# Kernel optimization log

Measured on AMD Instinct MI355X. Metric: run time of the kernel, lower is better.

## Reference

```python
import jax, jax.numpy as jnp
import numpy as np

HIDDEN = 1024
N_HEADS = 16
HEAD_DIM = HIDDEN // N_HEADS


def setup_inputs() -> dict:
    key = jax.random.key(0)
    ks = jax.random.split(key, 8)
    bs, seq = 8, 1024
    hidden_states = jax.random.normal(ks[0], (bs, seq, HIDDEN), dtype=jnp.float32)
    attention_mask = jnp.zeros((bs, 1, 1, seq), dtype=jnp.float32)
    s = 1.0 / np.sqrt(HIDDEN)
    Wq = jax.random.normal(ks[1], (HIDDEN, HIDDEN), dtype=jnp.float32) * s
    bq = jnp.zeros((HIDDEN,), dtype=jnp.float32)
    Wk = jax.random.normal(ks[2], (HIDDEN, HIDDEN), dtype=jnp.float32) * s
    bk = jnp.zeros((HIDDEN,), dtype=jnp.float32)
    Wv = jax.random.normal(ks[3], (HIDDEN, HIDDEN), dtype=jnp.float32) * s
    bv = jnp.zeros((HIDDEN,), dtype=jnp.float32)
    return {"hidden_states": hidden_states, "attention_mask": attention_mask,
            "Wq": Wq, "bq": bq, "Wk": Wk, "bk": bk, "Wv": Wv, "bv": bv}


def _split_heads(x):
    # [b, s, H] -> [b, h, s, d]
    b, s, _ = x.shape
    return x.reshape(b, s, N_HEADS, HEAD_DIM).transpose(0, 2, 1, 3)


def reference(hidden_states, attention_mask, Wq, bq, Wk, bk, Wv, bv):
    q = _split_heads(hidden_states @ Wq.T + bq)
    k = _split_heads(hidden_states @ Wk.T + bk)
    v = _split_heads(hidden_states @ Wv.T + bv)
    scale = 1.0 / np.sqrt(HEAD_DIM).astype(np.float32)
    scores = jnp.einsum('bhqd,bhkd->bhqk', q, k) * scale + attention_mask
    probs = jax.nn.softmax(scores, axis=-1)  # dropout p=0.0 -> identity
    ctx = jnp.einsum('bhqk,bhkd->bhqd', probs, v)
    b, h, s, d = ctx.shape
    return ctx.transpose(0, 2, 1, 3).reshape(b, s, h * d)
```

## Files before the change

kernel.cpp:

```cpp
#include <hip/hip_runtime.h>
#include <stdint.h>
#include <stddef.h>

#define HIDDEN 1024
#define NHEADS 16
#define HDIM   64
#define BS     8
#define SEQ    1024
#define MTOT   (BS*SEQ)
#define QKV_T  ((size_t)MTOT*HIDDEN)

typedef short    bf16x8 __attribute__((ext_vector_type(8)));
typedef short    bf16x4 __attribute__((ext_vector_type(4)));
typedef float    f32x4  __attribute__((ext_vector_type(4)));
typedef uint16_t u16x4  __attribute__((ext_vector_type(4)));

__device__ __forceinline__ uint16_t f2bf(float f) {
  union { float f; uint32_t u; } c; c.f = f;
  uint32_t u = c.u + 0x7FFFu + ((c.u >> 16) & 1u);
  return (uint16_t)(u >> 16);
}

__device__ __forceinline__ uint32_t cvt_pk_bf16(float lo, float hi) {
  uint32_t r;
  asm("v_cvt_pk_bf16_f32 %0, %1, %2" : "=v"(r) : "v"(lo), "v"(hi));
  return r;
}

__device__ __forceinline__ bf16x4 pack_bf16x4(float a, float b, float c, float d) {
  union { uint2 u; bf16x4 v; } cv;
  cv.u.x = cvt_pk_bf16(a, b);
  cv.u.y = cvt_pk_bf16(c, d);
  return cv.v;
}

__device__ __forceinline__ f32x4 mfma_16x16x16(bf16x4 a, bf16x4 b, f32x4 c) {
#if __has_builtin(__builtin_amdgcn_mfma_f32_16x16x16bf16_1k)
  return __builtin_amdgcn_mfma_f32_16x16x16bf16_1k(a, b, c, 0, 0, 0);
#elif __has_builtin(__builtin_amdgcn_mfma_f32_16x16x16_bf16)
  return __builtin_amdgcn_mfma_f32_16x16x16_bf16(a, b, c, 0, 0, 0);
#else
  f32x4 d;
  asm("v_mfma_f32_16x16x16_bf16 %0, %1, %2, %3"
      : "=&v"(d) : "v"(a), "v"(b), "v"(c));
  return d;
#endif
}

__device__ __forceinline__ float exp2fast(float x) {
#if __has_builtin(__builtin_amdgcn_exp2f)
  return __builtin_amdgcn_exp2f(x);
#else
  return __expf(x * 0.69314718056f);
#endif
}

__device__ __forceinline__ void gload_lds16(const uint16_t* g, uint16_t* lds) {
  __builtin_amdgcn_global_load_lds(
      (const __attribute__((address_space(1))) uint32_t*)g,
      (__attribute__((address_space(3))) uint32_t*)lds, 16, 0, 0);
}

__global__ __launch_bounds__(256) void cvt_kernel(
    const float* __restrict__ hs, const float* __restrict__ wq,
    const float* __restrict__ wk, const float* __restrict__ wv,
    uint16_t* __restrict__ hsb, uint16_t* __restrict__ wcat)
{
  const int i4 = blockIdx.x * 256 + threadIdx.x;
  f32x4 v;
  u16x4 o;
  if (i4 < 2097152) {
    v = *((const f32x4*)hs + i4);
    o[0]=f2bf(v[0]); o[1]=f2bf(v[1]); o[2]=f2bf(v[2]); o[3]=f2bf(v[3]);
    *((u16x4*)hsb + i4) = o;
  } else {
    int j4 = i4 - 2097152;
    int w  = j4 >> 18;
    int r4 = j4 & 262143;
    const float* src = (w == 0) ? wq : ((w == 1) ? wk : wv);
    v = *((const f32x4*)src + r4);
    o[0]=f2bf(v[0]); o[1]=f2bf(v[1]); o[2]=f2bf(v[2]); o[3]=f2bf(v[3]);
    *((u16x4*)wcat + j4) = o;
  }
}

__global__ __launch_bounds__(256) void gemm_qkv(
    const uint16_t* __restrict__ hsb, const uint16_t* __restrict__ wcat,
    const float* __restrict__ bq, const float* __restrict__ bk,
    const float* __restrict__ bv, uint16_t* __restrict__ qbuf,
    uint16_t* __restrict__ kbuf, uint16_t* __restrict__ vtbuf)
{
  __shared__ uint16_t Alds[2][128*32];
  __shared__ uint16_t Blds[2][128*32];

  const int bid = blockIdx.x;
  const int wg  = (bid & 7) * 192 + (bid >> 3);
  const int tm  = wg / 24, tn = wg % 24;
  const int m0  = tm * 128, n0 = tn * 128;
  const int t   = threadIdx.x;
  const int l   = t & 63, w = t >> 6;
  const int wm  = w >> 1, wn = w & 1;

  f32x4 acc[4][4];
#pragma unroll
  for (int i = 0; i < 4; i++)
#pragma unroll
    for (int j = 0; j < 4; j++) acc[i][j] = (f32x4){0.f,0.f,0.f,0.f};

  const int r0   = (w * 2) * 16 + (l >> 2);
  const int r1   = (w * 2 + 1) * 16 + (l >> 2);
  const int g0s  = (l & 3) ^ ((r0 >> 1) & 3);
  const int g1s  = (l & 3) ^ ((r1 >> 1) & 3);
  const size_t aoff0 = (size_t)r0 * HIDDEN + g0s * 8;
  const size_t aoff1 = (size_t)r1 * HIDDEN + g1s * 8;

  auto STAGE = [&](int buf, int kt) {
    const uint16_t* Ab = hsb  + (size_t)m0 * HIDDEN + kt * 32;
    const uint16_t* Bb = wcat + (size_t)n0 * HIDDEN + kt * 32;
    gload_lds16(Ab + aoff0, &Alds[buf][(w * 2) * 512]);
    gload_lds16(Ab + aoff1, &Alds[buf][(w * 2 + 1) * 512]);
    gload_lds16(Bb + aoff0, &Blds[buf][(w * 2) * 512]);
    gload_lds16(Bb + aoff1, &Blds[buf][(w * 2 + 1) * 512]);
  };

  auto COMPUTE = [&](int buf) {
    bf16x8 af[4], bfr[4];
    const int G = l >> 4;
#pragma unroll
    for (int i = 0; i < 4; i++) {
      int ar = wm * 64 + i * 16 + (l & 15);
      int gs = (G ^ ((ar >> 1) & 3)) & 3;
      af[i] = *(const bf16x8*)&Alds[buf][ar * 32 + gs * 8];
    }
#pragma unroll
    for (int j = 0; j < 4; j++) {
      int br = wn * 64 + j * 16 + (l & 15);
      int gs = (G ^ ((br >> 1) & 3)) & 3;
      bfr[j] = *(const bf16x8*)&Blds[buf][br * 32 + gs * 8];
    }
#pragma unroll
    for (int i = 0; i < 4; i++)
#pragma unroll
      for (int j = 0; j < 4; j++)
        acc[i][j] = __builtin_amdgcn_mfma_f32_16x16x32_bf16(af[i], bfr[j], acc[i][j], 0, 0, 0);
  };

  STAGE(0, 0);
  STAGE(1, 1);
#pragma unroll 1
  for (int kt = 0; kt < 32; ++kt) {
    if (kt < 31) { asm volatile("s_waitcnt vmcnt(4)" ::: "memory"); }
    else         { asm volatile("s_waitcnt vmcnt(0)" ::: "memory"); }
    __builtin_amdgcn_s_barrier();
    __builtin_amdgcn_sched_barrier(0);
    COMPUTE(kt & 1);
    if (kt < 31) {
      __builtin_amdgcn_s_barrier();
      __builtin_amdgcn_sched_barrier(0);
      if (kt < 30) STAGE(kt & 1, kt + 2);
    }
  }

#pragma unroll
  for (int j = 0; j < 4; j++) {
    int n     = n0 + wn * 64 + j * 16 + (l & 15);
    int which = n >> 10, nn = n & 1023;
    const float* bp = (which == 0) ? bq : ((which == 1) ? bk : bv);
    float bias = bp[nn];
    int hh = nn >> 6, dd = nn & 63;
#pragma unroll
    for (int i = 0; i < 4; i++) {
      if (which == 2) {
        int m_  = m0 + wm * 64 + i * 16 + (l >> 4) * 4;
        int b_  = m_ >> 10, s_ = m_ & 1023;
        size_t bhh = (size_t)(b_ * NHEADS + hh);
        uint2 pk;
        pk.x = cvt_pk_bf16(acc[i][j][0] + bias, acc[i][j][1] + bias);
        pk.y = cvt_pk_bf16(acc[i][j][2] + bias, acc[i][j][3] + bias);
        *(uint2*)&vtbuf[(bhh * HDIM + dd) * SEQ + s_] = pk;
      } else {
#pragma unroll
        for (int r = 0; r < 4; r++) {
          int m  = m0 + wm * 64 + i * 16 + (l >> 4) * 4 + r;
          int b_ = m >> 10, s_ = m & 1023;
          float val = acc[i][j][r] + bias;
          size_t bhh = (size_t)(b_ * NHEADS + hh);
          if (which == 0)
            qbuf[(bhh * SEQ + s_) * HDIM + dd] = f2bf(val * 0.18033688011112042f);
          else
            kbuf[(bhh * SEQ + s_) * HDIM + dd] = f2bf(val);
        }
      }
    }
  }
}

__global__ __launch_bounds__(256) void attn_kernel(
    const uint16_t* __restrict__ qb, const uint16_t* __restrict__ kb,
    const uint16_t* __restrict__ vtb, const float* __restrict__ mask,
    float* __restrict__ out)
{
  __shared__ uint16_t Klds[128 * 64];
  __shared__ uint16_t Vlds[64 * 128];
  __shared__ float    mlds[SEQ];

  const int bid = blockIdx.x;
  const int wg  = (bid & 7) * 128 + (bid >> 3);
  const int bh  = wg >> 3;
  const int qt  = wg & 7;
  const int b   = bh >> 4, h = bh & 15;

  const uint16_t* Qg = qb  + (size_t)bh * SEQ * HDIM;
  const uint16_t* Kg = kb  + (size_t)bh * SEQ * HDIM;
  const uint16_t* Vg = vtb + (size_t)bh * HDIM * SEQ;

  const int t = threadIdx.x, l = t & 63, w = t >> 6;
  const int G = l >> 4, q16 = l & 15;

  for (int i = t; i < SEQ; i += 256)
    mlds[i] = mask[b * SEQ + i] * 1.44269504089f;

  const int q0w = qt * 128 + w * 32;
  bf16x8 qf[2][2];
#pragma unroll
  for (int qi = 0; qi < 2; ++qi)
#pragma unroll
    for (int k0 = 0; k0 < 2; ++k0)
      qf[qi][k0] = *(const bf16x8*)(Qg + (size_t)(q0w + qi * 16 + q16) * HDIM + k0 * 32 + G * 8);

  f32x4 O0[4], O1[4];
#pragma unroll
  for (int dt = 0; dt < 4; dt++) { O0[dt] = (f32x4){0,0,0,0}; O1[dt] = (f32x4){0,0,0,0}; }
  float mrow0 = -3e38f, mrow1 = -3e38f, lrow0 = 0.f, lrow1 = 0.f;

  const int srow8 = l >> 3;
  const int gsrcK = (l & 7) ^ srow8;
  const int qsw = q16 & 7;

  auto softmax_q = [&](f32x4 (&scq)[8], bf16x4 (&paq)[8], float& mq, float& lq,
                       f32x4 (&Oq)[4], int ktbase) {
    float pm = -3e38f;
#pragma unroll
    for (int jn = 0; jn < 8; jn++) {
      f32x4 mvj = *(const f32x4*)&mlds[ktbase + jn * 16 + G * 4];
      scq[jn] += mvj;
      pm = fmaxf(pm, fmaxf(fmaxf(scq[jn][0], scq[jn][1]), fmaxf(scq[jn][2], scq[jn][3])));
    }
    pm = fmaxf(pm, __shfl_xor(pm, 16));
    pm = fmaxf(pm, __shfl_xor(pm, 32));
    if (!__all(pm <= mq + 11.0f)) {
      float mn = fmaxf(mq, pm);
      float fs = exp2fast(mq - mn);
      mq = mn; lq *= fs;
#pragma unroll
      for (int dt = 0; dt < 4; dt++) Oq[dt] *= fs;
    }
    float ps = 0.f;
#pragma unroll
    for (int jn = 0; jn < 8; jn++) {
      float p0 = exp2fast(scq[jn][0] - mq);
      float p1 = exp2fast(scq[jn][1] - mq);
      float p2 = exp2fast(scq[jn][2] - mq);
      float p3 = exp2fast(scq[jn][3] - mq);
      ps += (p0 + p1) + (p2 + p3);
      paq[jn] = pack_bf16x4(p0, p1, p2, p3);
    }
    ps += __shfl_xor(ps, 16);
    ps += __shfl_xor(ps, 32);
    lq += ps;
  };

  __syncthreads();

#pragma unroll 1
  for (int kt = 0; kt < 8; ++kt) {
    const int ktbase = kt * 128;
#pragma unroll
    for (int ja = 0; ja < 4; ja++) {
      const int rbK = ja * 32 + w * 8;
      gload_lds16(Kg + (size_t)(ktbase + rbK + srow8) * HDIM + gsrcK * 8,
                  &Klds[rbK * 64]);
      const int rbV = ja * 16 + w * 4;
      const int dV  = rbV + (l >> 4);
      const int gV  = (l & 15) ^ (dV & 7);
      gload_lds16(Vg + (size_t)dV * SEQ + ktbase + gV * 8,
                  &Vlds[rbV * 128]);
    }
    __syncthreads();

    f32x4 sc0[8], sc1[8];
#pragma unroll
    for (int jn = 0; jn < 8; jn++) {
      const int kr  = jn * 16 + q16;
      const int gs0 = (G ^ qsw) & 7;
      const int gs1 = ((4 + G) ^ qsw) & 7;
      bf16x8 kf0 = *(const bf16x8*)&Klds[kr * 64 + gs0 * 8];
      bf16x8 kf1 = *(const bf16x8*)&Klds[kr * 64 + gs1 * 8];
      f32x4 z = (f32x4){0, 0, 0, 0};
      sc0[jn] = __builtin_amdgcn_mfma_f32_16x16x32_bf16(kf0, qf[0][0], z, 0, 0, 0);
      sc0[jn] = __builtin_amdgcn_mfma_f32_16x16x32_bf16(kf1, qf[0][1], sc0[jn], 0, 0, 0);
      sc1[jn] = __builtin_amdgcn_mfma_f32_16x16x32_bf16(kf0, qf[1][0], z, 0, 0, 0);
      sc1[jn] = __builtin_amdgcn_mfma_f32_16x16x32_bf16(kf1, qf[1][1], sc1[jn], 0, 0, 0);
    }

    bf16x4 pa0[8], pa1[8];
    softmax_q(sc0, pa0, mrow0, lrow0, O0, ktbase);
    softmax_q(sc1, pa1, mrow1, lrow1, O1, ktbase);

#pragma unroll
    for (int jn = 0; jn < 8; jn++) {
      const int gq = 2 * jn + (G >> 1);
#pragma unroll
      for (int dt = 0; dt < 4; dt++) {
        const int dr   = dt * 16 + q16;
        const int slot = gq ^ (dr & 7);
        bf16x4 vf = *(const bf16x4*)&Vlds[dr * 128 + slot * 8 + (G & 1) * 4];
        O0[dt] = mfma_16x16x16(vf, pa0[jn], O0[dt]);
        O1[dt] = mfma_16x16x16(vf, pa1[jn], O1[dt]);
      }
    }
    __syncthreads();
  }

  {
    float inv0 = 1.0f / lrow0, inv1 = 1.0f / lrow1;
    int qa = q0w + q16, qb2 = q0w + 16 + q16;
    float* orow0 = out + (size_t)(b * SEQ + qa)  * HIDDEN + h * HDIM;
    float* orow1 = out + (size_t)(b * SEQ + qb2) * HIDDEN + h * HDIM;
#pragma unroll
    for (int dt = 0; dt < 4; dt++) {
      f32x4 a = O0[dt] * inv0;
      f32x4 c = O1[dt] * inv1;
      *(f32x4*)(orow0 + dt * 16 + G * 4) = a;
      *(f32x4*)(orow1 + dt * 16 + G * 4) = c;
    }
  }
}

extern "C" void kernel_launch(void* const* d_in, const int* in_sizes, int n_in,
                              void* d_out, int out_size, void* d_ws, size_t ws_size,
                              hipStream_t stream) {
  const float* hs   = (const float*)d_in[0];
  const float* mask = (const float*)d_in[1];
  const float* Wq   = (const float*)d_in[2];
  const float* bq   = (const float*)d_in[3];
  const float* Wk   = (const float*)d_in[4];
  const float* bk   = (const float*)d_in[5];
  const float* Wv   = (const float*)d_in[6];
  const float* bv   = (const float*)d_in[7];
  float* out = (float*)d_out;

  uint16_t* hsb  = (uint16_t*)d_ws;
  uint16_t* wcat = (uint16_t*)((char*)d_ws + 16777216u);
  uint16_t* qbuf = (uint16_t*)((char*)d_ws + 23068672u);
  uint16_t* kbuf = (uint16_t*)((char*)d_ws + 39845888u);
  uint16_t* vtbf = (uint16_t*)((char*)d_ws + 56623104u);

  cvt_kernel<<<11264, 256, 0, stream>>>(hs, Wq, Wk, Wv, hsb, wcat);
  gemm_qkv<<<1536, 256, 0, stream>>>(hsb, wcat, bq, bk, bv, qbuf, kbuf, vtbf);
  attn_kernel<<<1024, 256, 0, stream>>>(qbuf, kbuf, vtbf, mask, out);
}
```

Baseline: 144.6 us.

## Enlarge QKV GEMM tile to 256x128 with 512-thread blocks

```diff
diff --git a/kernel.cpp b/kernel.cpp
--- a/kernel.cpp
+++ b/kernel.cpp
@@ -84,22 +84,23 @@
   }
 }
 
-__global__ __launch_bounds__(256) void gemm_qkv(
+__global__ __launch_bounds__(512, 4) void gemm_qkv(
     const uint16_t* __restrict__ hsb, const uint16_t* __restrict__ wcat,
     const float* __restrict__ bq, const float* __restrict__ bk,
     const float* __restrict__ bv, uint16_t* __restrict__ qbuf,
     uint16_t* __restrict__ kbuf, uint16_t* __restrict__ vtbuf)
 {
-  __shared__ uint16_t Alds[2][128*32];
+  __shared__ uint16_t Alds[2][256*32];
   __shared__ uint16_t Blds[2][128*32];
 
   const int bid = blockIdx.x;
-  const int wg  = (bid & 7) * 192 + (bid >> 3);
+  const int wg  = (bid & 7) * 96 + (bid >> 3);
   const int tm  = wg / 24, tn = wg % 24;
-  const int m0  = tm * 128, n0 = tn * 128;
+  const int m0  = tm * 256, n0 = tn * 128;
   const int t   = threadIdx.x;
   const int l   = t & 63, w = t >> 6;
   const int wm  = w >> 1, wn = w & 1;
+  const int q16 = l & 15;
 
   f32x4 acc[4][4];
 #pragma unroll
@@ -107,20 +108,19 @@
 #pragma unroll
     for (int j = 0; j < 4; j++) acc[i][j] = (f32x4){0.f,0.f,0.f,0.f};
 
-  const int r0   = (w * 2) * 16 + (l >> 2);
-  const int r1   = (w * 2 + 1) * 16 + (l >> 2);
-  const int g0s  = (l & 3) ^ ((r0 >> 1) & 3);
-  const int g1s  = (l & 3) ^ ((r1 >> 1) & 3);
-  const size_t aoff0 = (size_t)r0 * HIDDEN + g0s * 8;
-  const size_t aoff1 = (size_t)r1 * HIDDEN + g1s * 8;
+  const int lrow = l >> 2;
+  const int rB   = w * 16 + lrow;
+  const int gsw  = (l & 3) ^ ((rB >> 1) & 3);
+  const size_t offA0 = (size_t)rB * HIDDEN + gsw * 8;
+  const size_t offA1 = (size_t)(128 + rB) * HIDDEN + gsw * 8;
+  const size_t offB  = offA0;
 
   auto STAGE = [&](int buf, int kt) {
     const uint16_t* Ab = hsb  + (size_t)m0 * HIDDEN + kt * 32;
     const uint16_t* Bb = wcat + (size_t)n0 * HIDDEN + kt * 32;
-    gload_lds16(Ab + aoff0, &Alds[buf][(w * 2) * 512]);
-    gload_lds16(Ab + aoff1, &Alds[buf][(w * 2 + 1) * 512]);
-    gload_lds16(Bb + aoff0, &Blds[buf][(w * 2) * 512]);
-    gload_lds16(Bb + aoff1, &Blds[buf][(w * 2 + 1) * 512]);
+    gload_lds16(Ab + offA0, &Alds[buf][(w * 16) * 32]);
+    gload_lds16(Ab + offA1, &Alds[buf][(128 + w * 16) * 32]);
+    gload_lds16(Bb + offB,  &Blds[buf][(w * 16) * 32]);
   };
 
   auto COMPUTE = [&](int buf) {
@@ -128,28 +128,30 @@
     const int G = l >> 4;
 #pragma unroll
     for (int i = 0; i < 4; i++) {
-      int ar = wm * 64 + i * 16 + (l & 15);
+      int ar = wm * 64 + i * 16 + q16;
       int gs = (G ^ ((ar >> 1) & 3)) & 3;
       af[i] = *(const bf16x8*)&Alds[buf][ar * 32 + gs * 8];
     }
 #pragma unroll
     for (int j = 0; j < 4; j++) {
-      int br = wn * 64 + j * 16 + (l & 15);
+      int br = wn * 64 + j * 16 + q16;
       int gs = (G ^ ((br >> 1) & 3)) & 3;
       bfr[j] = *(const bf16x8*)&Blds[buf][br * 32 + gs * 8];
     }
+    __builtin_amdgcn_s_setprio(1);
 #pragma unroll
     for (int i = 0; i < 4; i++)
 #pragma unroll
       for (int j = 0; j < 4; j++)
         acc[i][j] = __builtin_amdgcn_mfma_f32_16x16x32_bf16(af[i], bfr[j], acc[i][j], 0, 0, 0);
+    __builtin_amdgcn_s_setprio(0);
   };
 
   STAGE(0, 0);
   STAGE(1, 1);
 #pragma unroll 1
   for (int kt = 0; kt < 32; ++kt) {
-    if (kt < 31) { asm volatile("s_waitcnt vmcnt(4)" ::: "memory"); }
+    if (kt < 31) { asm volatile("s_waitcnt vmcnt(3)" ::: "memory"); }
     else         { asm volatile("s_waitcnt vmcnt(0)" ::: "memory"); }
     __builtin_amdgcn_s_barrier();
     __builtin_amdgcn_sched_barrier(0);
@@ -163,7 +165,7 @@
 
 #pragma unroll
   for (int j = 0; j < 4; j++) {
-    int n     = n0 + wn * 64 + j * 16 + (l & 15);
+    int n     = n0 + wn * 64 + j * 16 + q16;
     int which = n >> 10, nn = n & 1023;
     const float* bp = (which == 0) ? bq : ((which == 1) ? bk : bv);
     float bias = bp[nn];
@@ -357,6 +359,6 @@
   uint16_t* vtbf = (uint16_t*)((char*)d_ws + 56623104u);
 
   cvt_kernel<<<11264, 256, 0, stream>>>(hs, Wq, Wk, Wv, hsb, wcat);
-  gemm_qkv<<<1536, 256, 0, stream>>>(hsb, wcat, bq, bk, bv, qbuf, kbuf, vtbf);
+  gemm_qkv<<<768, 512, 0, stream>>>(hsb, wcat, bq, bk, bv, qbuf, kbuf, vtbf);
   attn_kernel<<<1024, 256, 0, stream>>>(qbuf, kbuf, vtbf, mask, out);
 }
```

After: 145.6 us. No clear change (+0.7%).
